# Performance work log

Hardware: AMD Instinct MI355X
Metric: run time of the kernel (lower is better)

Reference implementation:

```python
import jax, jax.numpy as jnp
import numpy as np

F, B, V, D = 26, 16384, 100000, 32  # features, batch, vocab per table, embed dim
H = F // 2  # SE-net hidden (reduction=2)


def setup_inputs() -> dict:
    key = jax.random.key(0)
    k1, k2, k3, k4 = jax.random.split(key, 4)
    x = jax.random.randint(k1, (F, B), 0, V, dtype=jnp.int32)
    emb_tables = jax.random.normal(k2, (F, V, D), dtype=jnp.float32) * 0.05
    w1 = jax.random.normal(k3, (H, F), dtype=jnp.float32) * 0.2  # fc1 weight [out,in]
    w2 = jax.random.normal(k4, (F, H), dtype=jnp.float32) * 0.2  # fc2 weight [out,in]
    return {"x": x, "emb_tables": emb_tables, "w1": w1, "w2": w2}


def reference(x, emb_tables, w1, w2):
    # Fused multi-table gather: [F, B, D]
    emb = jax.vmap(lambda table, idx: table[idx])(emb_tables, x)
    # SE-net input: per-feature mean over embedding dim -> [B, F]
    se_in = jnp.mean(emb, axis=-1).T
    h = jax.nn.relu(se_in @ w1.T)              # [B, H]
    gate = jax.nn.sigmoid(h @ w2.T)            # [B, F]
    # Faithful to original: scale every sample by the LAST batch row's gates
    scale = gate[-1]                            # [F]
    emb = emb * scale[:, None, None]
    # concat per-feature [B, D] blocks along dim 1 -> [B, F*D]
    out = jnp.transpose(emb, (1, 0, 2)).reshape(B, F * D)
    return out.astype(jnp.float32)
```

## Files before the change

kernel.cpp:

```cpp
#include <hip/hip_runtime.h>
#include <cmath>

constexpr int F = 26;
constexpr int B = 16384;
constexpr int V = 100000;
constexpr int D = 32;
constexpr int H = 13;

typedef float nfloat4 __attribute__((ext_vector_type(4)));

constexpr int F4_PER_B = F * D / 4;
constexpr int TOTAL_F4 = B * F4_PER_B;
constexpr int ITEMS    = 4;
constexpr int THREADS  = 256;
constexpr int SLICE    = TOTAL_F4 / ITEMS;
constexpr int GRID     = SLICE / THREADS;

__global__ __launch_bounds__(256) void fused_gather_se_kernel(
        const int* __restrict__ x,
        const float4* __restrict__ tables4,
        const float* __restrict__ w1,
        const float* __restrict__ w2,
        nfloat4* __restrict__ out4) {
    __shared__ float s_part[F * 8];
    __shared__ float s_se[F];
    __shared__ float s_h[H];
    __shared__ float s_scale[F];

    const int t = threadIdx.x;

    if (t < F * 8) {
        const int f  = t >> 3;
        const int d4 = t & 7;
        const int idx = x[f * B + (B - 1)];
        float4 v = tables4[(size_t)f * (V * D / 4) + (size_t)idx * (D / 4) + d4];
        s_part[t] = v.x + v.y + v.z + v.w;
    }
    __syncthreads();
    if (t < F) {
        float s = 0.0f;
#pragma unroll
        for (int j = 0; j < 8; ++j) s += s_part[t * 8 + j];
        s_se[t] = s * (1.0f / (float)D);
    }
    __syncthreads();
    if (t < H) {
        float a = 0.0f;
#pragma unroll
        for (int f = 0; f < F; ++f) a += w1[t * F + f] * s_se[f];
        s_h[t] = a > 0.0f ? a : 0.0f;
    }
    __syncthreads();
    if (t < F) {
        float a = 0.0f;
#pragma unroll
        for (int j = 0; j < H; ++j) a += w2[t * H + j] * s_h[j];
        s_scale[t] = 1.0f / (1.0f + expf(-a));
    }
    __syncthreads();

    const int tid = blockIdx.x * THREADS + t;

    int f[ITEMS], d4[ITEMS], bb[ITEMS];
#pragma unroll
    for (int k = 0; k < ITEMS; ++k) {
        const int g = tid + k * SLICE;
        const int b = g / F4_PER_B;
        const int r = g - b * F4_PER_B;
        f[k]  = r >> 3;
        d4[k] = r & 7;
        bb[k] = b;
    }

    int idx[ITEMS];
#pragma unroll
    for (int k = 0; k < ITEMS; ++k) idx[k] = x[f[k] * B + bb[k]];

    float4 v[ITEMS];
#pragma unroll
    for (int k = 0; k < ITEMS; ++k)
        v[k] = tables4[(size_t)f[k] * (V * D / 4) + (size_t)idx[k] * (D / 4) + d4[k]];

#pragma unroll
    for (int k = 0; k < ITEMS; ++k) {
        const float s = s_scale[f[k]];
        nfloat4 w;
        w.x = v[k].x * s; w.y = v[k].y * s;
        w.z = v[k].z * s; w.w = v[k].w * s;
        __builtin_nontemporal_store(w, &out4[tid + (size_t)k * SLICE]);
    }
}

extern "C" void kernel_launch(void* const* d_in, const int* in_sizes, int n_in,
                              void* d_out, int out_size, void* d_ws, size_t ws_size,
                              hipStream_t stream) {
    const int*   x      = (const int*)d_in[0];
    const float* tables = (const float*)d_in[1];
    const float* w1     = (const float*)d_in[2];
    const float* w2     = (const float*)d_in[3];
    float*       out    = (float*)d_out;

    fused_gather_se_kernel<<<GRID, THREADS, 0, stream>>>(
        x, (const float4*)tables, w1, w2, (nfloat4*)out);
}
```

Measured before the change: 401.4 us.

## Remap work to feature-major blocks with XCD-aware block swizzle

```diff
diff --git a/kernel.cpp b/kernel.cpp
--- a/kernel.cpp
+++ b/kernel.cpp
@@ -9,14 +9,14 @@
 
 typedef float nfloat4 __attribute__((ext_vector_type(4)));
 
-constexpr int F4_PER_B = F * D / 4;
-constexpr int TOTAL_F4 = B * F4_PER_B;
-constexpr int ITEMS    = 4;
-constexpr int THREADS  = 256;
-constexpr int SLICE    = TOTAL_F4 / ITEMS;
-constexpr int GRID     = SLICE / THREADS;
+constexpr int F4_PER_B   = F * D / 4;
+constexpr int THREADS    = 256;
+constexpr int ITEMS      = 4;
+constexpr int ROWS_PER_BLOCK = THREADS / 8 * ITEMS;
+constexpr int BLOCKS_PER_F   = B / ROWS_PER_BLOCK;
+constexpr int GRID           = F * BLOCKS_PER_F;
 
-__global__ __launch_bounds__(256) void fused_gather_se_kernel(
+__global__ __launch_bounds__(256) void fused_gather_se_fmajor(
         const int* __restrict__ x,
         const float4* __restrict__ tables4,
         const float* __restrict__ w1,
@@ -59,35 +59,34 @@
     }
     __syncthreads();
 
-    const int tid = blockIdx.x * THREADS + t;
+    const int bid  = blockIdx.x;
+    const int vbid = (bid & 7) * (GRID / 8) + (bid >> 3);
+    const int f     = vbid >> 7;
+    const int bbase = (vbid & 127) << 7;
 
-    int f[ITEMS], d4[ITEMS], bb[ITEMS];
-#pragma unroll
-    for (int k = 0; k < ITEMS; ++k) {
-        const int g = tid + k * SLICE;
-        const int b = g / F4_PER_B;
-        const int r = g - b * F4_PER_B;
-        f[k]  = r >> 3;
-        d4[k] = r & 7;
-        bb[k] = b;
-    }
+    const float s   = s_scale[f];
+    const int lane_d4    = t & 7;
+    const int row_in_blk = t >> 3;
+
+    const float4* __restrict__ tbase = tables4 + (size_t)f * (V * D / 4);
+    const int*    __restrict__ xf    = x + f * B + bbase;
 
     int idx[ITEMS];
 #pragma unroll
-    for (int k = 0; k < ITEMS; ++k) idx[k] = x[f[k] * B + bb[k]];
+    for (int k = 0; k < ITEMS; ++k) idx[k] = xf[row_in_blk + k * 32];
 
     float4 v[ITEMS];
 #pragma unroll
     for (int k = 0; k < ITEMS; ++k)
-        v[k] = tables4[(size_t)f[k] * (V * D / 4) + (size_t)idx[k] * (D / 4) + d4[k]];
+        v[k] = tbase[(size_t)idx[k] * (D / 4) + lane_d4];
 
 #pragma unroll
     for (int k = 0; k < ITEMS; ++k) {
-        const float s = s_scale[f[k]];
+        const int b = bbase + row_in_blk + k * 32;
         nfloat4 w;
         w.x = v[k].x * s; w.y = v[k].y * s;
         w.z = v[k].z * s; w.w = v[k].w * s;
-        __builtin_nontemporal_store(w, &out4[tid + (size_t)k * SLICE]);
+        __builtin_nontemporal_store(w, &out4[(size_t)b * F4_PER_B + f * 8 + lane_d4]);
     }
 }
 
@@ -100,6 +99,6 @@
     const float* w2     = (const float*)d_in[3];
     float*       out    = (float*)d_out;
 
-    fused_gather_se_kernel<<<GRID, THREADS, 0, stream>>>(
+    fused_gather_se_fmajor<<<GRID, THREADS, 0, stream>>>(
         x, (const float4*)tables, w1, w2, (nfloat4*)out);
 }
```

Result: no change. 399.0 us (-0.6%).
